# Kernel tuning notes

Hardware: AMD Instinct MI355X
Metric: run time of the kernel (lower is better)

## Reference

```python
import jax, jax.numpy as jnp
import numpy as np

WAY = 5
SHOT = 5
SCALE = 10.0
EPS = 1e-8


def setup_inputs() -> dict:
    key = jax.random.key(0)
    k1, k2 = jax.random.split(key, 2)
    x = jax.random.normal(k1, (100, 512, 16, 16), dtype=jnp.float32)
    W = jax.random.normal(k2, (512, 512), dtype=jnp.float32) * 0.02  # 1x1 conv weight (outC, inC)
    b = jnp.zeros((512,), dtype=jnp.float32)
    return {"x": x, "W": W, "b": b}


def reference(x, W, b):
    B, C, H, Wd = x.shape
    # extract(): 1x1 conv -> softmax over flattened (C*H*W) per sample -> remask
    mask = jnp.einsum('bchw,oc->bohw', x, W) + b[None, :, None, None]
    mask = jax.nn.softmax(mask.reshape(B, -1), axis=1).reshape(B, C, H, Wd)
    x = x * mask
    # predict(): (way, shot+query, C, H, W)
    xv = x.reshape(WAY, -1, C, H, Wd)
    s = xv[:, :SHOT].mean(axis=(1, 3, 4))                    # (m=way, d=C) support prototypes
    q = xv[:, SHOT:].reshape(-1, C, H * Wd)                  # (n, d=C, f=H*W) queries
    # cosine_similarity over d, without materializing (n,m,d,f)
    qn = jnp.maximum(jnp.sqrt(jnp.sum(q * q, axis=1)), EPS)  # (n, f)
    sn = jnp.maximum(jnp.sqrt(jnp.sum(s * s, axis=1)), EPS)  # (m,)
    scores = jnp.einsum('ndf,md->nmf', q, s) / (qn[:, None, :] * sn[None, :, None])
    # softmax over classes (m), then mean over spatial positions f
    return jax.nn.softmax(SCALE * scores, axis=1).mean(axis=2)  # (n, way)
```

## Files before the change

### kernel.cpp

```cpp
#include <hip/hip_runtime.h>
#include <hip/hip_bf16.h>
#include <math.h>

typedef _Float16 half8 __attribute__((ext_vector_type(8)));
typedef float f32x4 __attribute__((ext_vector_type(4)));

#define BATCH 100
#define CH    512
#define HWP   256
#define SAMP  (CH * HWP)

__device__ __forceinline__ void async16(const void* g, void* l) {
  __builtin_amdgcn_global_load_lds(
      (const __attribute__((address_space(1))) unsigned int*)g,
      (__attribute__((address_space(3))) unsigned int*)l, 16, 0, 0);
}

__global__ __launch_bounds__(256) void k_txpose(const float* __restrict__ x,
                                               _Float16* __restrict__ xh,
                                               const float* __restrict__ W,
                                               _Float16* __restrict__ Wh) {
  __shared__ float tb[64][69];
  int bid  = blockIdx.x;
  if (bid >= 3200) {
    int base = (bid - 3200) * 1024 + threadIdx.x;
#pragma unroll
    for (int j = 0; j < 4; j++) Wh[base + j * 256] = (_Float16)W[base + j * 256];
    return;
  }
  int b    = bid >> 5;
  int tile = bid & 31;
  int c0 = (tile >> 2) << 6;
  int p0 = (tile & 3) << 6;
  int t = threadIdx.x;
  const float* xb = x + (size_t)b * SAMP;
#pragma unroll
  for (int it = 0; it < 4; it++) {
    int ch = it * 256 + t;
    int c  = ch >> 4;
    int pc = (ch & 15) << 2;
    float4 v = *(const float4*)(xb + (size_t)(c0 + c) * HWP + p0 + pc);
    tb[c][pc] = v.x; tb[c][pc + 1] = v.y; tb[c][pc + 2] = v.z; tb[c][pc + 3] = v.w;
  }
  __syncthreads();
  _Float16* xhb = xh + (size_t)b * SAMP;
#pragma unroll
  for (int it = 0; it < 2; it++) {
    int ch = it * 256 + t;
    int p  = ch >> 3;
    int ck = (ch & 7) << 3;
    half8 h;
#pragma unroll
    for (int j = 0; j < 8; j++) h[j] = (_Float16)tb[ck + j][p];
    *(half8*)(xhb + (size_t)(p0 + p) * CH + c0 + ck) = h;
  }
}

__global__ __launch_bounds__(256) void k_gemm(const _Float16* __restrict__ Wh,
                                             const _Float16* __restrict__ xh,
                                             const float* __restrict__ bias,
                                             _Float16* __restrict__ u,
                                             float* __restrict__ denom) {
  __shared__ __align__(16) _Float16 smem[128 * 136];
  int bid = blockIdx.x;
  int w     = (bid & 7) * 100 + (bid >> 3);
  int batch = w >> 3;
  int sub   = w & 7;
  int ot = sub & 3, pt = sub >> 2;
  int o0 = ot * 128, p0 = pt * 128;
  const _Float16* Bg = xh + (size_t)batch * SAMP;

  int t  = threadIdx.x;
  int wv = t >> 6, ln = t & 63;
  int qd = ln >> 4, r = ln & 15;
  int wm0 = (wv >> 1) * 64, wn0 = (wv & 1) * 64;
  int slr = (qd ^ ((r >> 1) & 3)) << 3;

  _Float16* const A0 = smem;
  _Float16* const B0 = smem + 4096;
  _Float16* const A1 = smem + 8192;
  _Float16* const B1 = smem + 12288;

#define STAGE(As, Bs, kk)                                                     \
  {                                                                           \
    _Pragma("unroll")                                                         \
    for (int it = 0; it < 2; it++) {                                          \
      int ch  = it * 256 + t;                          \
      int row = ch >> 2;                                          \
      int qsw = (ch & 3) ^ ((row >> 1) & 3);    \
      char* la = (char*)(As) + (size_t)(it * 256 + wv * 64) * 16;             \
      char* lb = (char*)(Bs) + (size_t)(it * 256 + wv * 64) * 16;             \
      async16((const char*)(Wh + (size_t)(o0 + row) * 512 + (kk) + qsw * 8), la); \
      async16((const char*)(Bg + (size_t)(p0 + row) * 512 + (kk) + qsw * 8), lb); \
    }                                                                         \
  }

#define COMPUTE(As, Bs)                                                       \
  {                                                                           \
    half8 af[4], bf[4];                                                       \
    _Pragma("unroll")                                                         \
    for (int i = 0; i < 4; i++)                                               \
      af[i] = *(const half8*)((As) + (wm0 + i * 16 + r) * 32 + slr);          \
    _Pragma("unroll")                                                         \
    for (int j = 0; j < 4; j++)                                               \
      bf[j] = *(const half8*)((Bs) + (wn0 + j * 16 + r) * 32 + slr);          \
    _Pragma("unroll")                                                         \
    for (int i = 0; i < 4; i++)                                               \
      _Pragma("unroll")                                                       \
      for (int j = 0; j < 4; j++)                                             \
        acc[i][j] = __builtin_amdgcn_mfma_f32_16x16x32_f16(af[i], bf[j], acc[i][j], 0, 0, 0); \
  }

  f32x4 acc[4][4] = {};
  STAGE(A0, B0, 0);
  __syncthreads();

#pragma unroll 1
  for (int ks = 0; ks < 16; ks += 2) {
    STAGE(A1, B1, (ks + 1) * 32);
    COMPUTE(A0, B0);
    __syncthreads();
    if (ks < 14) STAGE(A0, B0, (ks + 2) * 32);
    COMPUTE(A1, B1);
    __syncthreads();
  }
#undef STAGE
#undef COMPUTE

#pragma unroll
  for (int it = 0; it < 8; it++) {
    int ch = it * 256 + t;
    int p  = ch >> 4;
    int ck = ch & 15;
    half8 v = *(const half8*)(Bg + (size_t)(p0 + p) * CH + o0 + ck * 8);
    *(half8*)(smem + p * 136 + ck * 8) = v;
  }
  __syncthreads();

  _Float16* outb = u + (size_t)batch * SAMP;
  float lsum = 0.f;
#pragma unroll
  for (int i = 0; i < 4; i++) {
#pragma unroll
    for (int rg = 0; rg < 4; rg++) {
      int ol = wm0 + i * 16 + qd * 4 + rg;
      float bv = bias[o0 + ol];
#pragma unroll
      for (int j = 0; j < 4; j++) {
        int pl = wn0 + j * 16 + r;
        float ev = __expf(acc[i][j][rg] + bv);
        lsum += ev;
        float xv = (float)smem[pl * 136 + ol];
        outb[(size_t)(o0 + ol) * HWP + p0 + pl] = (_Float16)(xv * ev);
      }
    }
  }
#pragma unroll
  for (int off = 32; off; off >>= 1) lsum += __shfl_down(lsum, off, 64);
  __shared__ float rs[4];
  if (ln == 0) rs[wv] = lsum;
  __syncthreads();
  if (t == 0) atomicAdd(&denom[batch], rs[0] + rs[1] + rs[2] + rs[3]);
}

__global__ __launch_bounds__(256) void k_proto(const _Float16* __restrict__ u,
                                              const float* __restrict__ denom,
                                              float* __restrict__ sproto) {
  int c = blockIdx.x;
  int t = threadIdx.x;
  int wv = t >> 6;
  float accm[5];
#pragma unroll
  for (int m = 0; m < 5; m++) {
    float acc = 0.f;
#pragma unroll
    for (int j = 0; j < 5; j++) {
      int b = m * 20 + j;
      acc += (float)u[(size_t)b * SAMP + (size_t)c * HWP + t] * (1.0f / denom[b]);
    }
    accm[m] = acc;
  }
#pragma unroll
  for (int m = 0; m < 5; m++) {
    float v = accm[m];
#pragma unroll
    for (int off = 32; off; off >>= 1) v += __shfl_down(v, off, 64);
    accm[m] = v;
  }
  __shared__ float rs[4][5];
  if ((t & 63) == 0) {
#pragma unroll
    for (int m = 0; m < 5; m++) rs[wv][m] = accm[m];
  }
  __syncthreads();
  if (t < 5) sproto[t * 512 + c] =
      (rs[0][t] + rs[1][t] + rs[2][t] + rs[3][t]) * (1.0f / 1280.0f);
}

__global__ __launch_bounds__(256) void k_sn(const float* __restrict__ sproto,
                                           float* __restrict__ pref) {
  int m = blockIdx.x, t = threadIdx.x;
  float v1 = sproto[m * 512 + t], v2 = sproto[m * 512 + 256 + t];
  float acc = v1 * v1 + v2 * v2;
#pragma unroll
  for (int off = 32; off; off >>= 1) acc += __shfl_down(acc, off, 64);
  __shared__ float rs[4];
  if ((t & 63) == 0) rs[t >> 6] = acc;
  __syncthreads();
  if (t == 0) {
    float sn = fmaxf(sqrtf(rs[0] + rs[1] + rs[2] + rs[3]), 1e-8f);
    pref[m] = 10.0f / sn;
  }
}

__global__ __launch_bounds__(256) void k_part(const _Float16* __restrict__ u,
                                             const float* __restrict__ sproto,
                                             float* __restrict__ part) {
  __shared__ float s_l[5 * 64];
  int n = blockIdx.x >> 3, gc = blockIdx.x & 7;
  int b = (n / 15) * 20 + 5 + (n % 15);
  int t = threadIdx.x;
  for (int i = t; i < 320; i += 256)
    s_l[i] = sproto[(i >> 6) * 512 + gc * 64 + (i & 63)];
  __syncthreads();
  const _Float16* ub = u + (size_t)b * SAMP + (size_t)gc * 64 * HWP;
  float dot[5] = {0, 0, 0, 0, 0}, qq = 0.f;
#pragma unroll 8
  for (int c = 0; c < 64; c++) {
    float v = (float)ub[c * HWP + t];
    qq += v * v;
#pragma unroll
    for (int m = 0; m < 5; m++) dot[m] += v * s_l[m * 64 + c];
  }
  float* pp = part + (size_t)(n * 8 + gc) * 6 * 256 + t;
  pp[0 * 256] = dot[0]; pp[1 * 256] = dot[1]; pp[2 * 256] = dot[2];
  pp[3 * 256] = dot[3]; pp[4 * 256] = dot[4]; pp[5 * 256] = qq;
}

__global__ __launch_bounds__(256) void k_comb(const float* __restrict__ part,
                                             const float* __restrict__ pref,
                                             float* __restrict__ out) {
  int n = blockIdx.x, t = threadIdx.x;
  float dot[5] = {0, 0, 0, 0, 0}, qq = 0.f;
#pragma unroll
  for (int gc = 0; gc < 8; gc++) {
    const float* pp = part + (size_t)(n * 8 + gc) * 6 * 256 + t;
    dot[0] += pp[0 * 256]; dot[1] += pp[1 * 256]; dot[2] += pp[2 * 256];
    dot[3] += pp[3 * 256]; dot[4] += pp[4 * 256]; qq += pp[5 * 256];
  }
  float iqn = 1.0f / fmaxf(sqrtf(qq), 1e-20f);
  float sc[5], mx = -1e30f;
#pragma unroll
  for (int m = 0; m < 5; m++) { sc[m] = dot[m] * pref[m] * iqn; mx = fmaxf(mx, sc[m]); }
  float p[5], ssum = 0.f;
#pragma unroll
  for (int m = 0; m < 5; m++) { p[m] = __expf(sc[m] - mx); ssum += p[m]; }
  float rr = 1.0f / ssum;
#pragma unroll
  for (int m = 0; m < 5; m++) {
    float v = p[m] * rr;
#pragma unroll
    for (int off = 32; off; off >>= 1) v += __shfl_down(v, off, 64);
    p[m] = v;
  }
  __shared__ float rs[4][5];
  if ((t & 63) == 0) {
#pragma unroll
    for (int m = 0; m < 5; m++) rs[t >> 6][m] = p[m];
  }
  __syncthreads();
  if (t < 5) out[n * 5 + t] =
      (rs[0][t] + rs[1][t] + rs[2][t] + rs[3][t]) * (1.0f / 256.0f);
}

extern "C" void kernel_launch(void* const* d_in, const int* in_sizes, int n_in,
                              void* d_out, int out_size, void* d_ws, size_t ws_size,
                              hipStream_t stream) {
  const float* x    = (const float*)d_in[0];
  const float* W    = (const float*)d_in[1];
  const float* bias = (const float*)d_in[2];
  float* out = (float*)d_out;

  char* ws = (char*)d_ws;
  _Float16* xh     = (_Float16*)(ws + 0);
  float*    part   = (float*)   (ws + 0);
  _Float16* Wh     = (_Float16*)(ws + 26214400);
  _Float16* u      = (_Float16*)(ws + 26738688);
  float*    denom  = (float*)   (ws + 52953088);
  float*    sproto = (float*)   (ws + 52953600);
  float*    pref   = (float*)   (ws + 52963840);

  hipMemsetAsync(denom, 0, 512, stream);
  k_txpose <<<3456, 256, 0, stream>>>(x, xh, W, Wh);
  k_gemm   <<<800,  256, 0, stream>>>(Wh, xh, bias, u, denom);
  k_proto  <<<512,  256, 0, stream>>>(u, denom, sproto);
  k_sn     <<<5,    256, 0, stream>>>(sproto, pref);
  k_part   <<<600,  256, 0, stream>>>(u, sproto, part);
  k_comb   <<<75,   256, 0, stream>>>(part, pref, out);
}
```

Measured before the change: 137.4 us.

## Pre-pack GEMM operands into MFMA fragment layout and load fragments directly from global

The transpose kernel now writes x and W in fp16 in a packed layout matching the 16x16x32 MFMA fragment order, so each lane reads its half8 fragment with one contiguous global load. The GEMM drops the LDS double-buffered staging and its per-step barriers, keeping register double buffering of fragments instead. LDS is used only for the x tile needed in the epilogue, loaded asynchronously with an XOR swizzle in place of padding. This removes LDS round trips and syncs from the main loop, but each wave now reads its operand fragments straight from global/L2, and tiles shared between waves are fetched more than once.

```diff
diff --git a/kernel.cpp b/kernel.cpp
--- a/kernel.cpp
+++ b/kernel.cpp
@@ -10,6 +10,7 @@
 #define HWP   256
 #define SAMP  (CH * HWP)
 
+
 __device__ __forceinline__ void async16(const void* g, void* l) {
   __builtin_amdgcn_global_load_lds(
       (const __attribute__((address_space(1))) unsigned int*)g,
@@ -17,15 +18,20 @@
 }
 
 __global__ __launch_bounds__(256) void k_txpose(const float* __restrict__ x,
-                                               _Float16* __restrict__ xh,
+                                               _Float16* __restrict__ xhp,
                                                const float* __restrict__ W,
-                                               _Float16* __restrict__ Wh) {
+                                               _Float16* __restrict__ Whp) {
   __shared__ float tb[64][69];
   int bid  = blockIdx.x;
   if (bid >= 3200) {
-    int base = (bid - 3200) * 1024 + threadIdx.x;
-#pragma unroll
-    for (int j = 0; j < 4; j++) Wh[base + j * 256] = (_Float16)W[base + j * 256];
+    int tid = (bid - 3200) * 256 + threadIdx.x;
+    int o  = tid >> 6, c8 = tid & 63;
+    const float* wp = W + (size_t)o * 512 + c8 * 8;
+    half8 h;
+#pragma unroll
+    for (int j = 0; j < 8; j++) h[j] = (_Float16)wp[j];
+    *(half8*)(Whp + (size_t)((o >> 4) * 16 + (c8 >> 2)) * 512
+              + ((o & 15) + ((c8 & 3) << 4)) * 8) = h;
     return;
   }
   int b    = bid >> 5;
@@ -43,98 +49,85 @@
     tb[c][pc] = v.x; tb[c][pc + 1] = v.y; tb[c][pc + 2] = v.z; tb[c][pc + 3] = v.w;
   }
   __syncthreads();
-  _Float16* xhb = xh + (size_t)b * SAMP;
+  _Float16* xhb = xhp + (size_t)b * SAMP;
 #pragma unroll
   for (int it = 0; it < 2; it++) {
     int ch = it * 256 + t;
     int p  = ch >> 3;
-    int ck = (ch & 7) << 3;
+    int c8 = ch & 7;
     half8 h;
 #pragma unroll
-    for (int j = 0; j < 8; j++) h[j] = (_Float16)tb[ck + j][p];
-    *(half8*)(xhb + (size_t)(p0 + p) * CH + c0 + ck) = h;
-  }
-}
-
-__global__ __launch_bounds__(256) void k_gemm(const _Float16* __restrict__ Wh,
-                                             const _Float16* __restrict__ xh,
+    for (int j = 0; j < 8; j++) h[j] = (_Float16)tb[c8 * 8 + j][p];
+    int pg  = p0 + p;
+    int c8g = (c0 >> 3) + c8;
+    *(half8*)(xhb + (size_t)((pg >> 4) * 16 + (c8g >> 2)) * 512
+              + ((pg & 15) + ((c8g & 3) << 4)) * 8) = h;
+  }
+}
+
+__global__ __launch_bounds__(256) void k_gemm(const _Float16* __restrict__ Whp,
+                                             const _Float16* __restrict__ xhp,
                                              const float* __restrict__ bias,
                                              _Float16* __restrict__ u,
                                              float* __restrict__ denom) {
-  __shared__ __align__(16) _Float16 smem[128 * 136];
+  __shared__ __align__(16) _Float16 smem[128 * 128];
+  __shared__ float rs[4];
   int bid = blockIdx.x;
   int w     = (bid & 7) * 100 + (bid >> 3);
   int batch = w >> 3;
   int sub   = w & 7;
   int ot = sub & 3, pt = sub >> 2;
   int o0 = ot * 128, p0 = pt * 128;
-  const _Float16* Bg = xh + (size_t)batch * SAMP;
+  const _Float16* Xb = xhp + (size_t)batch * SAMP;
 
   int t  = threadIdx.x;
   int wv = t >> 6, ln = t & 63;
   int qd = ln >> 4, r = ln & 15;
   int wm0 = (wv >> 1) * 64, wn0 = (wv & 1) * 64;
-  int slr = (qd ^ ((r >> 1) & 3)) << 3;
-
-  _Float16* const A0 = smem;
-  _Float16* const B0 = smem + 4096;
-  _Float16* const A1 = smem + 8192;
-  _Float16* const B1 = smem + 12288;
-
-#define STAGE(As, Bs, kk)                                                     \
-  {                                                                           \
-    _Pragma("unroll")                                                         \
-    for (int it = 0; it < 2; it++) {                                          \
-      int ch  = it * 256 + t;                          \
-      int row = ch >> 2;                                          \
-      int qsw = (ch & 3) ^ ((row >> 1) & 3);    \
-      char* la = (char*)(As) + (size_t)(it * 256 + wv * 64) * 16;             \
-      char* lb = (char*)(Bs) + (size_t)(it * 256 + wv * 64) * 16;             \
-      async16((const char*)(Wh + (size_t)(o0 + row) * 512 + (kk) + qsw * 8), la); \
-      async16((const char*)(Bg + (size_t)(p0 + row) * 512 + (kk) + qsw * 8), lb); \
-    }                                                                         \
-  }
-
-#define COMPUTE(As, Bs)                                                       \
-  {                                                                           \
-    half8 af[4], bf[4];                                                       \
-    _Pragma("unroll")                                                         \
+
+  const _Float16* Ab = Whp + (size_t)((o0 + wm0) >> 4) * 16 * 512 + ln * 8;
+  const _Float16* Bb = Xb  + (size_t)((p0 + wn0) >> 4) * 16 * 512 + ln * 8;
+
+#define LOADF(aa, bb, ks)                                                     \
+  { _Pragma("unroll")                                                         \
     for (int i = 0; i < 4; i++)                                               \
-      af[i] = *(const half8*)((As) + (wm0 + i * 16 + r) * 32 + slr);          \
+      aa[i] = *(const half8*)(Ab + (size_t)(i * 16 + (ks)) * 512);            \
     _Pragma("unroll")                                                         \
     for (int j = 0; j < 4; j++)                                               \
-      bf[j] = *(const half8*)((Bs) + (wn0 + j * 16 + r) * 32 + slr);          \
-    _Pragma("unroll")                                                         \
+      bb[j] = *(const half8*)(Bb + (size_t)(j * 16 + (ks)) * 512); }
+
+#define MFMA16(aa, bb)                                                        \
+  { _Pragma("unroll")                                                         \
     for (int i = 0; i < 4; i++)                                               \
       _Pragma("unroll")                                                       \
       for (int j = 0; j < 4; j++)                                             \
-        acc[i][j] = __builtin_amdgcn_mfma_f32_16x16x32_f16(af[i], bf[j], acc[i][j], 0, 0, 0); \
-  }
+        acc[i][j] = __builtin_amdgcn_mfma_f32_16x16x32_f16(aa[i], bb[j], acc[i][j], 0, 0, 0); }
 
   f32x4 acc[4][4] = {};
-  STAGE(A0, B0, 0);
-  __syncthreads();
-
-#pragma unroll 1
+  half8 a0[4], b0[4], a1[4], b1[4];
+  LOADF(a0, b0, 0);
+
+#pragma unroll
+  for (int it = 0; it < 8; it++) {
+    int s   = it * 256 + t;
+    int p   = s >> 4, lc8 = s & 15;
+    int pg  = p0 + p;
+    int c8g = (o0 >> 3) + (lc8 ^ (p & 7));
+    const _Float16* src = Xb + (size_t)((pg >> 4) * 16 + (c8g >> 2)) * 512
+                             + ((pg & 15) + ((c8g & 3) << 4)) * 8;
+    async16(src, smem + (size_t)(it * 256 + wv * 64) * 8);
+  }
+
+#pragma unroll
   for (int ks = 0; ks < 16; ks += 2) {
-    STAGE(A1, B1, (ks + 1) * 32);
-    COMPUTE(A0, B0);
-    __syncthreads();
-    if (ks < 14) STAGE(A0, B0, (ks + 2) * 32);
-    COMPUTE(A1, B1);
-    __syncthreads();
-  }
-#undef STAGE
-#undef COMPUTE
-
-#pragma unroll
-  for (int it = 0; it < 8; it++) {
-    int ch = it * 256 + t;
-    int p  = ch >> 4;
-    int ck = ch & 15;
-    half8 v = *(const half8*)(Bg + (size_t)(p0 + p) * CH + o0 + ck * 8);
-    *(half8*)(smem + p * 136 + ck * 8) = v;
-  }
+    LOADF(a1, b1, ks + 1);
+    MFMA16(a0, b0);
+    if (ks < 14) LOADF(a0, b0, ks + 2);
+    MFMA16(a1, b1);
+  }
+#undef LOADF
+#undef MFMA16
+
   __syncthreads();
 
   _Float16* outb = u + (size_t)batch * SAMP;
@@ -145,19 +138,19 @@
     for (int rg = 0; rg < 4; rg++) {
       int ol = wm0 + i * 16 + qd * 4 + rg;
       float bv = bias[o0 + ol];
+      int lo = ol >> 3, wo = ol & 7;
 #pragma unroll
       for (int j = 0; j < 4; j++) {
         int pl = wn0 + j * 16 + r;
         float ev = __expf(acc[i][j][rg] + bv);
         lsum += ev;
-        float xv = (float)smem[pl * 136 + ol];
+        float xv = (float)smem[pl * 128 + ((lo ^ (pl & 7)) << 3) + wo];
         outb[(size_t)(o0 + ol) * HWP + p0 + pl] = (_Float16)(xv * ev);
       }
     }
   }
 #pragma unroll
   for (int off = 32; off; off >>= 1) lsum += __shfl_down(lsum, off, 64);
-  __shared__ float rs[4];
   if (ln == 0) rs[wv] = lsum;
   __syncthreads();
   if (t == 0) atomicAdd(&denom[batch], rs[0] + rs[1] + rs[2] + rs[3]);
@@ -282,17 +275,17 @@
   float* out = (float*)d_out;
 
   char* ws = (char*)d_ws;
-  _Float16* xh     = (_Float16*)(ws + 0);
+  _Float16* xhp    = (_Float16*)(ws + 0);
   float*    part   = (float*)   (ws + 0);
-  _Float16* Wh     = (_Float16*)(ws + 26214400);
+  _Float16* Whp    = (_Float16*)(ws + 26214400);
   _Float16* u      = (_Float16*)(ws + 26738688);
   float*    denom  = (float*)   (ws + 52953088);
   float*    sproto = (float*)   (ws + 52953600);
   float*    pref   = (float*)   (ws + 52963840);
 
   hipMemsetAsync(denom, 0, 512, stream);
-  k_txpose <<<3456, 256, 0, stream>>>(x, xh, W, Wh);
-  k_gemm   <<<800,  256, 0, stream>>>(Wh, xh, bias, u, denom);
+  k_txpose <<<3328, 256, 0, stream>>>(x, xhp, W, Whp);
+  k_gemm   <<<800,  256, 0, stream>>>(Whp, xhp, bias, u, denom);
   k_proto  <<<512,  256, 0, stream>>>(u, denom, sproto);
   k_sn     <<<5,    256, 0, stream>>>(sproto, pref);
   k_part   <<<600,  256, 0, stream>>>(u, sproto, part);
```

Result: slower. 158.1 us (+15.1%).
